# Optimization experiments

Hardware: AMD Instinct MI355X
Metric: run time of the kernel (lower is better)

## Reference

```python
import jax, jax.numpy as jnp
import numpy as np

B, XL, YL = 4, 128, 1024
D, H, L, DFF = 512, 8, 3, 2048
PV, AV, OV = 512, 1025, 1025
MASK_ID = 1024
EOS = 1024
DUR_W = 1.0
NEG = -1e9  # finite large-negative instead of -inf: keeps fully-padded rows NaN-free
HD = D // H
S = XL + 1 + YL


def sinusoid(n, d):
    pos = jnp.arange(n, dtype=jnp.float32)[:, None]
    div = jnp.exp(jnp.arange(0, d, 2, dtype=jnp.float32) * (-np.log(10000.0) / d))
    pe = jnp.zeros((n, d), dtype=jnp.float32)
    pe = pe.at[:, 0::2].set(jnp.sin(pos * div))
    pe = pe.at[:, 1::2].set(jnp.cos(pos * div))
    return pe


def layer_norm(x, g, b, eps=1e-5):
    mu = x.mean(-1, keepdims=True)
    var = ((x - mu) ** 2).mean(-1, keepdims=True)
    return (x - mu) * jax.lax.rsqrt(var + eps) * g + b


def setup_inputs():
    k = jax.random.split(jax.random.key(0), 32)
    x = jax.random.randint(k[0], (B, XL), 0, PV)
    x1_lens = jax.random.randint(k[1], (B,), 20, 60)
    x2_lens = jax.random.randint(k[2], (B,), 20, 60)
    y = jax.random.randint(k[3], (B, YL), 0, AV - 2)
    y1_lens = jax.random.randint(k[4], (B,), 100, 400)
    y2_lens = jax.random.randint(k[5], (B,), 300, 600)
    y_lens = y1_lens + 1 + y2_lens
    idx = jnp.arange(YL)[None, :]
    valid = (idx >= y1_lens[:, None] + 1) & (idx < y_lens[:, None] - 1)
    bern = jax.random.uniform(k[6], (B, YL)) < 0.3  # mask_ratio = mid(min,max)
    ym = bern & valid
    need = (~ym.any(1)) & valid.any(1)
    first = jnp.argmax(valid, axis=1)
    y_mask = ym | (need[:, None] & (idx == first[:, None]))
    emo_feature = jax.random.normal(k[7], (B, 768), dtype=jnp.float32)

    def n(kk, shape, s=0.02):
        return s * jax.random.normal(kk, shape, dtype=jnp.float32)

    inp = dict(x=x, x1_lens=x1_lens, x2_lens=x2_lens, y=y, y1_lens=y1_lens,
               y2_lens=y2_lens, y_mask=y_mask, emo_feature=emo_feature)
    inp['text_emb'] = n(k[8], (PV, D))
    inp['audio_emb'] = n(k[9], (AV, D))
    inp['type_emb'] = n(k[10], (3, D))
    inp['emo_W'] = n(k[11], (D, 768))
    inp['emo_b'] = jnp.zeros((D,), jnp.float32)
    inp['alpha_text'] = jnp.float32(1.0)
    inp['alpha_audio'] = jnp.float32(1.0)
    inp['Wqkv'] = n(k[12], (L, 3 * D, D))
    inp['bqkv'] = jnp.zeros((L, 3 * D), jnp.float32)
    inp['Wo'] = n(k[13], (L, D, D))
    inp['bo'] = jnp.zeros((L, D), jnp.float32)
    inp['ln1_g'] = jnp.ones((L, D), jnp.float32)
    inp['ln1_b'] = jnp.zeros((L, D), jnp.float32)
    inp['ln2_g'] = jnp.ones((L, D), jnp.float32)
    inp['ln2_b'] = jnp.zeros((L, D), jnp.float32)
    inp['W1'] = n(k[14], (L, DFF, D))
    inp['b1'] = jnp.zeros((L, DFF), jnp.float32)
    inp['W2'] = n(k[15], (L, D, DFF))
    inp['b2'] = jnp.zeros((L, D), jnp.float32)
    inp['predict_W'] = n(k[16], (OV, D))
    inp['dW1'] = n(k[17], (D // 2, D))
    inp['db1'] = jnp.zeros((D // 2,), jnp.float32)
    inp['dW2'] = n(k[18], (D // 4, D // 2))
    inp['db2'] = jnp.zeros((D // 4,), jnp.float32)
    inp['dW3'] = n(k[19], (1, D // 4))
    inp['db3'] = jnp.zeros((1,), jnp.float32)
    return inp


def build_attn_bias(x1_lens, x2_lens, y1_lens, y2_lens, y_mask):
    x_lens = x1_lens + 1 + x2_lens
    y_lens = y1_lens + 1 + y2_lens
    cS = jnp.arange(S)[None, :]  # [1,S] key columns
    # --- x rows ---
    rx = jnp.arange(XL)[None, :]
    is_x1 = rx < x1_lens[:, None]                                   # [B,XL]
    allow_x1 = cS < x1_lens[:, None]                                # [B,S]
    allow_x2 = (cS >= x1_lens[:, None]) & (cS < x_lens[:, None])
    x_allow = jnp.where(is_x1[:, :, None], allow_x1[:, None, :], allow_x2[:, None, :])
    # --- emo row: attends only to itself (col XL) ---
    emo_allow = jnp.broadcast_to((cS == XL)[:, None, :], (B, 1, S))
    # --- y rows ---
    ry = jnp.arange(YL)[None, :]
    is_y1 = ry < y1_lens[:, None]
    is_cls = ry == y1_lens[:, None]
    is_y2 = (ry > y1_lens[:, None]) & (ry < y_lens[:, None])
    allow_y1 = (cS < x1_lens[:, None]) | ((cS > XL) & (cS <= XL + y1_lens[:, None]))
    allow_cls = (cS < x_lens[:, None]) | (cS == XL) | ((cS > XL) & (cS <= XL + y1_lens[:, None] + 1))
    allow_y2 = (cS < x_lens[:, None]) | (cS == XL) | ((cS > XL) & (cS <= XL + y_lens[:, None]))
    ymask_full = jnp.zeros((B, S), bool).at[:, XL + 1:].set(y_mask)
    allow_y2 = allow_y2 & (~ymask_full)                             # masked tokens invisible
    y_allow = jnp.where(is_y1[:, :, None], allow_y1[:, None, :],
               jnp.where(is_cls[:, :, None], allow_cls[:, None, :],
                jnp.where(is_y2[:, :, None], allow_y2[:, None, :], False)))
    block = ~jnp.concatenate([x_allow, emo_allow, y_allow], axis=1)  # True = blocked
    return jnp.where(block, jnp.float32(NEG), jnp.float32(0.0))[:, None]  # [B,1,S,S]


def encoder_forward(h, bias, Wqkv, bqkv, Wo, bo, ln1_g, ln1_b, ln2_g, ln2_b, W1, b1, W2, b2):
    scale = 1.0 / np.sqrt(HD)
    for l in range(L):
        qkv = h @ Wqkv[l].T + bqkv[l]                               # [B,S,3D]
        q, k, v = jnp.split(qkv, 3, axis=-1)
        q = q.reshape(B, S, H, HD).transpose(0, 2, 1, 3)
        k = k.reshape(B, S, H, HD).transpose(0, 2, 1, 3)
        v = v.reshape(B, S, H, HD).transpose(0, 2, 1, 3)
        scores = jnp.einsum('bhqd,bhkd->bhqk', q, k) * scale + bias
        a = jax.nn.softmax(scores, axis=-1)
        o = jnp.einsum('bhqk,bhkd->bhqd', a, v).transpose(0, 2, 1, 3).reshape(B, S, D)
        o = o @ Wo[l].T + bo[l]
        h = layer_norm(h + o, ln1_g[l], ln1_b[l])                   # post-norm
        ff = jax.nn.relu(h @ W1[l].T + b1[l]) @ W2[l].T + b2[l]
        h = layer_norm(h + ff, ln2_g[l], ln2_b[l])
    return h


def reference(x, x1_lens, x2_lens, y, y1_lens, y2_lens, y_mask, emo_feature,
              text_emb, audio_emb, type_emb, emo_W, emo_b, alpha_text, alpha_audio,
              Wqkv, bqkv, Wo, bo, ln1_g, ln1_b, ln2_g, ln2_b, W1, b1, W2, b2,
              predict_W, dW1, db1, dW2, db2, dW3, db3):
    y_target = y
    x_emb = text_emb[x] + type_emb[0]
    x_pos = x_emb + alpha_text * sinusoid(XL, D)
    emo = emo_feature @ emo_W.T + emo_b + type_emb[1]
    y_in = jnp.where(y_mask, MASK_ID, y)
    y_emb = audio_emb[y_in] + type_emb[2]
    y_pos = y_emb + alpha_audio * sinusoid(YL, D)
    h_input = jnp.concatenate([x_pos, emo[:, None, :], y_pos], axis=1)  # [B,S,D]
    bias = build_attn_bias(x1_lens, x2_lens, y1_lens, y2_lens, y_mask)
    enc = encoder_forward(h_input, bias, Wqkv, bqkv, Wo, bo,
                          ln1_g, ln1_b, ln2_g, ln2_b, W1, b1, W2, b2)
    # duration loss on CLS hidden at prompt_lens = XL + 1 + y1_lens
    cls_hidden = enc[jnp.arange(B), XL + 1 + y1_lens]
    h1 = jax.nn.relu(cls_hidden @ dW1.T + db1)
    h2 = jax.nn.relu(h1 @ dW2.T + db2)
    pred_dur = (h2 @ dW3.T + db3)[:, 0]
    tgt_dur = y2_lens.astype(jnp.float32) / x2_lens.astype(jnp.float32)
    e = pred_dur - tgt_dur
    dur_loss = jnp.mean(jnp.where(jnp.abs(e) <= 1.0, 0.5 * e * e, jnp.abs(e) - 0.5))
    # token CE over masked positions (mean over masked tokens)
    logits = enc[:, XL + 1:] @ predict_W.T                          # [B,YL,OV]
    logp = jax.nn.log_softmax(logits, axis=-1)
    ce = -jnp.take_along_axis(logp, y_target[..., None], axis=-1)[..., 0]
    m = y_mask.astype(jnp.float32)
    token_loss = jnp.sum(ce * m) / jnp.sum(m)
    # top-3 accuracy ignoring EOS
    top3 = jax.lax.top_k(logits, 3)[1]
    correct = jnp.any(top3 == y_target[..., None], axis=-1)
    inc = (y_mask & (y_target != EOS)).astype(jnp.float32)
    acc = jnp.sum(correct.astype(jnp.float32) * inc) / jnp.maximum(jnp.sum(inc), 1.0)
    total_loss = token_loss + DUR_W * dur_loss
    return total_loss, acc
```

## Files before the change

### kernel.cpp

```cpp
#include <hip/hip_runtime.h>
#include <hip/hip_bf16.h>
#include <math.h>

#define BATCH 4
#define XL 128
#define YL 1024
#define DMODEL 512
#define NH 8
#define NLAYER 3
#define DFF 2048
#define MASK_ID 1024
#define EOS_TOK 1024
#define HD 64
#define SEQ 1153
#define OV 1025
#define NEGBIG (-1e9f)
#define QBLK 128
#define CCAP 2432
#define NROWS 36896

typedef unsigned short u16;
typedef unsigned int u32;
typedef short short8 __attribute__((ext_vector_type(8)));
typedef float f32x4 __attribute__((ext_vector_type(4)));

__device__ __forceinline__ u16 f2bf(float f) {
    union { float f; unsigned u; } v; v.f = f;
    unsigned r = v.u + 0x7fffu + ((v.u >> 16) & 1u);
    return (u16)(r >> 16);
}
__device__ __forceinline__ float bf2f(u16 b) {
    union { unsigned u; float f; } v; v.u = ((unsigned)b) << 16;
    return v.f;
}

__global__ __launch_bounds__(256) void cvt5_kernel(
    const float* __restrict__ s0, u16* __restrict__ d0, int n0,
    const float* __restrict__ s1, u16* __restrict__ d1, int n1,
    const float* __restrict__ s2, u16* __restrict__ d2, int n2,
    const float* __restrict__ s3, u16* __restrict__ d3, int n3,
    const float* __restrict__ s4, u16* __restrict__ d4, int n4)
{
    int c0 = n0, c1 = c0 + n1, c2 = c1 + n2, c3 = c2 + n3, c4 = c3 + n4;
    for (int i = blockIdx.x * 256 + threadIdx.x; i < c4; i += gridDim.x * 256) {
        const float* s; u16* d; int j;
        if (i < c0)      { s = s0; d = d0; j = i; }
        else if (i < c1) { s = s1; d = d1; j = i - c0; }
        else if (i < c2) { s = s2; d = d2; j = i - c1; }
        else if (i < c3) { s = s3; d = d3; j = i - c2; }
        else             { s = s4; d = d4; j = i - c3; }
        float4 v = ((const float4*)s)[j];
        ushort4 o;
        o.x = f2bf(v.x); o.y = f2bf(v.y); o.z = f2bf(v.z); o.w = f2bf(v.w);
        ((ushort4*)d)[j] = o;
    }
}

__global__ __launch_bounds__(256) void emo_kernel(
    const float* __restrict__ emo_feature, const float* __restrict__ emo_W,
    const float* __restrict__ emo_b, const float* __restrict__ type_emb,
    float* __restrict__ hbuf, u16* __restrict__ hbuf_bf)
{
    int b = blockIdx.x >> 3, c = blockIdx.x & 7;
    int t = threadIdx.x;
    int osub = t >> 2, ln = t & 3;
    int d = c * 64 + osub;
    const float* f = emo_feature + b * 768 + ln * 192;
    const float* w = emo_W + (size_t)d * 768 + ln * 192;
    float acc = 0.f;
    #pragma unroll 4
    for (int k = 0; k < 192; ++k) acc = fmaf(f[k], w[k], acc);
    acc += __shfl_xor(acc, 1);
    acc += __shfl_xor(acc, 2);
    if (ln == 0) {
        float v = acc + emo_b[d] + type_emb[DMODEL + d];
        hbuf[(size_t)(b * SEQ + XL) * DMODEL + d] = v;
        hbuf_bf[(size_t)(b * SEQ + XL) * DMODEL + d] = f2bf(v);
    }
}

__global__ __launch_bounds__(256) void build_h_kernel(
    const int* __restrict__ x, const int* __restrict__ y, const int* __restrict__ y_mask,
    const float* __restrict__ text_emb, const float* __restrict__ audio_emb,
    const float* __restrict__ type_emb,
    const float* __restrict__ alpha_text, const float* __restrict__ alpha_audio,
    float* __restrict__ hbuf, u16* __restrict__ hbuf_bf)
{
    int row = blockIdx.x * 4 + (threadIdx.x >> 6);
    int l = threadIdx.x & 63;
    int b = row / SEQ, s = row % SEQ;
    if (s == XL) return;
    int d0 = l * 8;

    const float* emb; const float* te; float alpha; int pos;
    if (s < XL) {
        int tok = x[b * XL + s];
        emb = text_emb + (size_t)tok * DMODEL;
        te = type_emb; alpha = alpha_text[0]; pos = s;
    } else {
        int r = s - XL - 1;
        int tok = y_mask[b * YL + r] ? MASK_ID : y[b * YL + r];
        emb = audio_emb + (size_t)tok * DMODEL;
        te = type_emb + 2 * DMODEL; alpha = alpha_audio[0]; pos = r;
    }

    float4 e0 = *(const float4*)(emb + d0);
    float4 e1 = *(const float4*)(emb + d0 + 4);
    float4 t0 = *(const float4*)(te + d0);
    float4 t1 = *(const float4*)(te + d0 + 4);
    float v[8] = {e0.x + t0.x, e0.y + t0.y, e0.z + t0.z, e0.w + t0.w,
                  e1.x + t1.x, e1.y + t1.y, e1.z + t1.z, e1.w + t1.w};
    float fp = (float)pos;
    #pragma unroll
    for (int p = 0; p < 4; ++p) {
        int d = d0 + 2 * p;
        float div = __expf((float)d * (-9.210340371976184f / (float)DMODEL));
        float sn, cs;
        __sincosf(fp * div, &sn, &cs);
        v[2 * p]     += alpha * sn;
        v[2 * p + 1] += alpha * cs;
    }

    float* hp = hbuf + (size_t)row * DMODEL + d0;
    *(float4*)hp       = make_float4(v[0], v[1], v[2], v[3]);
    *(float4*)(hp + 4) = make_float4(v[4], v[5], v[6], v[7]);
    short8 sv;
    #pragma unroll
    for (int e = 0; e < 8; ++e) sv[e] = (short)f2bf(v[e]);
    *(short8*)(hbuf_bf + (size_t)row * DMODEL + d0) = sv;
}

__global__ __launch_bounds__(512) void gemm_bf16_kernel(
    const u16* __restrict__ A, const u16* __restrict__ Bw,
    const float* __restrict__ bias,
    float* __restrict__ Cf, u16* __restrict__ Cb,
    int M, int N, int K, int relu)
{
    __shared__ u16 As[128 * 32];
    __shared__ u16 Bs[128 * 32];
    int tid = threadIdx.x;
    int w = tid >> 6, l = tid & 63;
    int m0 = blockIdx.y * 128, n0 = blockIdx.x * 128;
    int wm = (w >> 1) * 32, wn = (w & 1) * 64;

    f32x4 acc[2][4];
    #pragma unroll
    for (int i = 0; i < 2; ++i)
        #pragma unroll
        for (int j = 0; j < 4; ++j) acc[i][j] = (f32x4){0.f, 0.f, 0.f, 0.f};

    int srow = (w << 4) + (l >> 2);
    int skp = (l & 3) << 3;

    for (int k0 = 0; k0 < K; k0 += 32) {
        {
            int am = m0 + srow; if (am >= M) am = M - 1;
            int bn = n0 + srow; if (bn >= N) bn = N - 1;
            __builtin_amdgcn_global_load_lds(
                (const __attribute__((address_space(1))) void*)(A + (size_t)am * K + k0 + skp),
                (__attribute__((address_space(3))) void*)(As + (w << 9)), 16, 0, 0);
            __builtin_amdgcn_global_load_lds(
                (const __attribute__((address_space(1))) void*)(Bw + (size_t)bn * K + k0 + skp),
                (__attribute__((address_space(3))) void*)(Bs + (w << 9)), 16, 0, 0);
        }
        __syncthreads();
        short8 af[2], bfr[4];
        #pragma unroll
        for (int i = 0; i < 2; ++i)
            af[i]  = *(const short8*)(As + (wm + i * 16 + (l & 15)) * 32 + ((l >> 4) << 3));
        #pragma unroll
        for (int j = 0; j < 4; ++j)
            bfr[j] = *(const short8*)(Bs + (wn + j * 16 + (l & 15)) * 32 + ((l >> 4) << 3));
        #pragma unroll
        for (int i = 0; i < 2; ++i)
            #pragma unroll
            for (int j = 0; j < 4; ++j)
                acc[i][j] = __builtin_amdgcn_mfma_f32_16x16x32_bf16(af[i], bfr[j], acc[i][j], 0, 0, 0);
        __syncthreads();
    }

    #pragma unroll
    for (int i = 0; i < 2; ++i) {
        #pragma unroll
        for (int j = 0; j < 4; ++j) {
            #pragma unroll
            for (int jj = 0; jj < 4; ++jj) {
                int row = m0 + wm + i * 16 + ((l >> 4) << 2) + jj;
                int col = n0 + wn + j * 16 + (l & 15);
                if (row < M && col < N) {
                    float v = acc[i][j][jj];
                    if (bias) v += bias[col];
                    if (relu) v = fmaxf(v, 0.f);
                    if (Cf) Cf[(size_t)row * N + col] = v;
                    if (Cb) Cb[(size_t)row * N + col] = f2bf(v);
                }
            }
        }
    }
}

__global__ __launch_bounds__(512) void gemm_bf16_splitk_kernel(
    const u16* __restrict__ A, const u16* __restrict__ Bw,
    float* __restrict__ P0, float* __restrict__ P1, float* __restrict__ P2,
    int M, int N, int K, int klen)
{
    __shared__ u16 As[128 * 32];
    __shared__ u16 Bs[128 * 32];
    int tid = threadIdx.x;
    int w = tid >> 6, l = tid & 63;
    int z = blockIdx.z;
    float* Cp = (z == 0) ? P0 : (z == 1) ? P1 : P2;
    int kbeg = z * klen;
    int kend = min(kbeg + klen, K);
    int m0 = blockIdx.y * 128, n0 = blockIdx.x * 128;
    int wm = (w >> 1) * 32, wn = (w & 1) * 64;

    f32x4 acc[2][4];
    #pragma unroll
    for (int i = 0; i < 2; ++i)
        #pragma unroll
        for (int j = 0; j < 4; ++j) acc[i][j] = (f32x4){0.f, 0.f, 0.f, 0.f};

    int srow = (w << 4) + (l >> 2);
    int skp = (l & 3) << 3;

    for (int k0 = kbeg; k0 < kend; k0 += 32) {
        {
            int am = m0 + srow; if (am >= M) am = M - 1;
            int bn = n0 + srow; if (bn >= N) bn = N - 1;
            __builtin_amdgcn_global_load_lds(
                (const __attribute__((address_space(1))) void*)(A + (size_t)am * K + k0 + skp),
                (__attribute__((address_space(3))) void*)(As + (w << 9)), 16, 0, 0);
            __builtin_amdgcn_global_load_lds(
                (const __attribute__((address_space(1))) void*)(Bw + (size_t)bn * K + k0 + skp),
                (__attribute__((address_space(3))) void*)(Bs + (w << 9)), 16, 0, 0);
        }
        __syncthreads();
        short8 af[2], bfr[4];
        #pragma unroll
        for (int i = 0; i < 2; ++i)
            af[i]  = *(const short8*)(As + (wm + i * 16 + (l & 15)) * 32 + ((l >> 4) << 3));
        #pragma unroll
        for (int j = 0; j < 4; ++j)
            bfr[j] = *(const short8*)(Bs + (wn + j * 16 + (l & 15)) * 32 + ((l >> 4) << 3));
        #pragma unroll
        for (int i = 0; i < 2; ++i)
            #pragma unroll
            for (int j = 0; j < 4; ++j)
                acc[i][j] = __builtin_amdgcn_mfma_f32_16x16x32_bf16(af[i], bfr[j], acc[i][j], 0, 0, 0);
        __syncthreads();
    }

    #pragma unroll
    for (int i = 0; i < 2; ++i) {
        #pragma unroll
        for (int j = 0; j < 4; ++j) {
            #pragma unroll
            for (int jj = 0; jj < 4; ++jj) {
                int row = m0 + wm + i * 16 + ((l >> 4) << 2) + jj;
                int col = n0 + wn + j * 16 + (l & 15);
                if (row < M && col < N)
                    Cp[(size_t)row * N + col] = acc[i][j][jj];
            }
        }
    }
}

__global__ __launch_bounds__(512) void gemm_bf16_splitk_dynm_kernel(
    const u16* __restrict__ A, const u16* __restrict__ Bw,
    const int* __restrict__ Mp,
    float* __restrict__ P0, float* __restrict__ P1,
    int N, int K, int klen)
{
    int M = *Mp;
    int m0 = blockIdx.y * 128;
    if (m0 >= M) return;
    __shared__ u16 As[128 * 32];
    __shared__ u16 Bs[128 * 32];
    int tid = threadIdx.x;
    int w = tid >> 6, l = tid & 63;
    int z = blockIdx.z;
    float* Cp = (z == 0) ? P0 : P1;
    int kbeg = z * klen;
    int kend = min(kbeg + klen, K);
    int n0 = blockIdx.x * 128;
    int wm = (w >> 1) * 32, wn = (w & 1) * 64;

    f32x4 acc[2][4];
    #pragma unroll
    for (int i = 0; i < 2; ++i)
        #pragma unroll
        for (int j = 0; j < 4; ++j) acc[i][j] = (f32x4){0.f, 0.f, 0.f, 0.f};

    int srow = (w << 4) + (l >> 2);
    int skp = (l & 3) << 3;

    for (int k0 = kbeg; k0 < kend; k0 += 32) {
        {
            int am = m0 + srow; if (am >= M) am = M - 1;
            int bn = n0 + srow; if (bn >= N) bn = N - 1;
            __builtin_amdgcn_global_load_lds(
                (const __attribute__((address_space(1))) void*)(A + (size_t)am * K + k0 + skp),
                (__attribute__((address_space(3))) void*)(As + (w << 9)), 16, 0, 0);
            __builtin_amdgcn_global_load_lds(
                (const __attribute__((address_space(1))) void*)(Bw + (size_t)bn * K + k0 + skp),
                (__attribute__((address_space(3))) void*)(Bs + (w << 9)), 16, 0, 0);
        }
        __syncthreads();
        short8 af[2], bfr[4];
        #pragma unroll
        for (int i = 0; i < 2; ++i)
            af[i]  = *(const short8*)(As + (wm + i * 16 + (l & 15)) * 32 + ((l >> 4) << 3));
        #pragma unroll
        for (int j = 0; j < 4; ++j)
            bfr[j] = *(const short8*)(Bs + (wn + j * 16 + (l & 15)) * 32 + ((l >> 4) << 3));
        #pragma unroll
        for (int i = 0; i < 2; ++i)
            #pragma unroll
            for (int j = 0; j < 4; ++j)
                acc[i][j] = __builtin_amdgcn_mfma_f32_16x16x32_bf16(af[i], bfr[j], acc[i][j], 0, 0, 0);
        __syncthreads();
    }

    #pragma unroll
    for (int i = 0; i < 2; ++i) {
        #pragma unroll
        for (int j = 0; j < 4; ++j) {
            #pragma unroll
            for (int jj = 0; jj < 4; ++jj) {
                int row = m0 + wm + i * 16 + ((l >> 4) << 2) + jj;
                int col = n0 + wn + j * 16 + (l & 15);
                if (row < M && col < N)
                    Cp[(size_t)row * N + col] = acc[i][j][jj];
            }
        }
    }
}

__global__ __launch_bounds__(512) void attn_mfma_kernel(
    const u16* __restrict__ qkv,
    const int* __restrict__ x1_lens, const int* __restrict__ x2_lens,
    const int* __restrict__ y1_lens, const int* __restrict__ y2_lens,
    const int* __restrict__ y_mask,
    float* __restrict__ opart, float* __restrict__ ml)
{
    __shared__ u16 Ks[64 * 64];
    __shared__ u16 Vt[64 * 64];
    __shared__ unsigned long long Bits[7][19];

    int tid = threadIdx.x;
    int w = tid >> 6, l = tid & 63;
    int g = l >> 4;
    int q = l & 15;
    int bh = blockIdx.y;
    int b = bh >> 3, h = bh & 7;
    int q0 = blockIdx.x * QBLK;
    int z = blockIdx.z;

    int x1 = x1_lens[b], xlen = x1 + 1 + x2_lens[b];
    int y1 = y1_lens[b], ylen = y1 + 1 + y2_lens[b];

    int kmax = -1;
    if (q0 < XL) kmax = max(kmax, xlen - 1);
    if (XL >= q0 && XL < q0 + QBLK) kmax = max(kmax, XL);
    {
        int ry0 = max(0, q0 - XL - 1);
        int ry1 = min(YL - 1, q0 + QBLK - 2 - XL);
        if (ry0 <= ry1) {
            if (ry0 <= y1 - 1) kmax = max(kmax, XL + y1);
            if (y1 >= ry0 && y1 <= ry1) kmax = max(kmax, XL + y1 + 1);
            int a = max(ry0, y1 + 1), bb = min(ry1, ylen - 1);
            if (a <= bb) kmax = max(kmax, XL + ylen);
        }
    }
    if (kmax < 0) kmax = 0;
    int NKT = (kmax >> 6) + 1;
    int half = (NKT + 1) >> 1;
    int kbeg = z ? half : 0;
    int kend = z ? NKT : half;

    for (int pp = w; pp < 7 * 19; pp += 8) {
        int ty = pp / 19, tile = pp - ty * 19;
        int c = tile * 64 + l;
        bool allow = false;
        if (c < SEQ && ty < 6) {
            bool a2c = (c == XL), ygt = (c > XL);
            if (ty == 0) allow = (c < x1);
            else if (ty == 1) allow = (c >= x1) && (c < xlen);
            else if (ty == 2) allow = a2c;
            else if (ty == 3) allow = (c < x1) || (ygt && c <= XL + y1);
            else if (ty == 4) allow = (c < xlen) || a2c || (ygt && c <= XL + y1 + 1);
            else {
                int ym = ygt ? y_mask[b * YL + c - XL - 1] : 0;
                allow = (((c < xlen) || a2c || (ygt && c <= XL + ylen)) && !ym);
            }
        }
        unsigned long long mk = __ballot(allow);
        if (l == 0) Bits[ty][tile] = mk;
    }

    int qr = q0 + w * 16 + q;
    int qrc = min(qr, SEQ - 1);
    short8 qf0, qf1;
    {
        const u16* qp = qkv + (size_t)(b * SEQ + qrc) * 1536 + h * 64 + (g << 3);
        short8 r0 = *(const short8*)qp;
        short8 r1 = *(const short8*)(qp + 32);
        #pragma unroll
        for (int e = 0; e < 8; ++e) {
            qf0[e] = (short)f2bf(bf2f((u16)r0[e]) * 0.125f);
            qf1[e] = (short)f2bf(bf2f((u16)r1[e]) * 0.125f);
        }
    }

    int rt;
    {
        if (qr >= SEQ) rt = 6;
        else if (qr < XL) rt = (qr < x1) ? 0 : 1;
        else if (qr == XL) rt = 2;
        else {
            int ry = qr - XL - 1;
            rt = (ry < y1) ? 3 : (ry == y1) ? 4 : (ry < ylen) ? 5 : 6;
        }
    }

    f32x4 oacc[4];
    #pragma unroll
    for (int db = 0; db < 4; ++db) oacc[db] = (f32x4){0.f, 0.f, 0.f, 0.f};
    float mrun = -INFINITY, lrun = 0.f;

    int srcA = q + ((g & 1) << 5);
    int srcB = srcA + 16;
    bool hi = (g >> 1) & 1;

    for (int kt = kbeg; kt < kend; ++kt) {
        __syncthreads();
        {
            int r = tid >> 3, d0k = (tid & 7) << 3;
            int krc = min(kt * 64 + r, SEQ - 1);
            short8 ka = *(const short8*)(qkv + (size_t)(b * SEQ + krc) * 1536 + 512 + h * 64 + d0k);
            *(short8*)&Ks[r * 64 + (d0k ^ ((r & 7) << 3))] = ka;
        }
        {
            int rp = tid >> 4, o = tid & 15;
            int d0v = o * 4;
            int k0r = min(kt * 64 + 2 * rp, SEQ - 1);
            int k1r = min(kt * 64 + 2 * rp + 1, SEQ - 1);
            ushort4 va = *(const ushort4*)(qkv + (size_t)(b * SEQ + k0r) * 1536 + 1024 + h * 64 + d0v);
            ushort4 vb = *(const ushort4*)(qkv + (size_t)(b * SEQ + k1r) * 1536 + 1024 + h * 64 + d0v);
            u32 pv[4] = {(u32)va.x | ((u32)vb.x << 16), (u32)va.y | ((u32)vb.y << 16),
                         (u32)va.z | ((u32)vb.z << 16), (u32)va.w | ((u32)vb.w << 16)};
            #pragma unroll
            for (int e = 0; e < 4; ++e) {
                int d = d0v + e;
                *(u32*)&Vt[d * 64 + ((2 * rp) ^ ((d & 7) << 3))] = pv[e];
            }
        }
        __syncthreads();

        f32x4 sc[4];
        #pragma unroll
        for (int cb = 0; cb < 4; ++cb) {
            int krw = cb * 16 + q;
            int ksw = (krw & 7) << 3;
            short8 k0 = *(const short8*)&Ks[krw * 64 + ((g << 3) ^ ksw)];
            short8 k1 = *(const short8*)&Ks[krw * 64 + ((32 + (g << 3)) ^ ksw)];
            f32x4 zz = (f32x4){0.f, 0.f, 0.f, 0.f};
            zz = __builtin_amdgcn_mfma_f32_16x16x32_bf16(k0, qf0, zz, 0, 0, 0);
            sc[cb] = __builtin_amdgcn_mfma_f32_16x16x32_bf16(k1, qf1, zz, 0, 0, 0);
        }

        unsigned long long mb = Bits[rt][kt];
        #pragma unroll
        for (int cb = 0; cb < 4; ++cb) {
            unsigned nib = (unsigned)(mb >> (16 * cb + 4 * g)) & 0xFu;
            #pragma unroll
            for (int r = 0; r < 4; ++r)
                sc[cb][r] = ((nib >> r) & 1u) ? sc[cb][r] : NEGBIG;
        }

        float tmax = sc[0][0];
        #pragma unroll
        for (int cb = 0; cb < 4; ++cb)
            #pragma unroll
            for (int r = 0; r < 4; ++r) tmax = fmaxf(tmax, sc[cb][r]);
        tmax = fmaxf(tmax, __shfl_xor(tmax, 16));
        tmax = fmaxf(tmax, __shfl_xor(tmax, 32));
        float newm = fmaxf(mrun, tmax);
        float corr = __expf(mrun - newm);
        float p[4][4];
        float ps = 0.f;
        #pragma unroll
        for (int cb = 0; cb < 4; ++cb)
            #pragma unroll
            for (int r = 0; r < 4; ++r) {
                p[cb][r] = __expf(sc[cb][r] - newm);
                ps += p[cb][r];
            }
        ps += __shfl_xor(ps, 16);
        ps += __shfl_xor(ps, 32);
        lrun = lrun * corr + ps;
        mrun = newm;

        float cr[4];
        #pragma unroll
        for (int r = 0; r < 4; ++r) cr[r] = __shfl(corr, (g << 2) + r);
        #pragma unroll
        for (int db = 0; db < 4; ++db)
            #pragma unroll
            for (int r = 0; r < 4; ++r) oacc[db][r] *= cr[r];

        u32 P0[4], P1[4];
        #pragma unroll
        for (int cb = 0; cb < 4; ++cb) {
            P0[cb] = (u32)f2bf(p[cb][0]) | ((u32)f2bf(p[cb][1]) << 16);
            P1[cb] = (u32)f2bf(p[cb][2]) | ((u32)f2bf(p[cb][3]) << 16);
        }

        union { u32 u[4]; short8 s; } f1, f2;
        {
            u32 a0 = __shfl(P0[0], srcA), a1 = __shfl(P1[0], srcA);
            u32 a2 = __shfl(P0[0], srcB), a3 = __shfl(P1[0], srcB);
            u32 b0 = __shfl(P0[1], srcA), b1 = __shfl(P1[1], srcA);
            u32 b2 = __shfl(P0[1], srcB), b3 = __shfl(P1[1], srcB);
            f1.u[0] = hi ? b0 : a0; f1.u[1] = hi ? b1 : a1;
            f1.u[2] = hi ? b2 : a2; f1.u[3] = hi ? b3 : a3;
            u32 c0 = __shfl(P0[2], srcA), c1 = __shfl(P1[2], srcA);
            u32 c2 = __shfl(P0[2], srcB), c3 = __shfl(P1[2], srcB);
            u32 d0 = __shfl(P0[3], srcA), d1 = __shfl(P1[3], srcA);
            u32 d2 = __shfl(P0[3], srcB), d3 = __shfl(P1[3], srcB);
            f2.u[0] = hi ? d0 : c0; f2.u[1] = hi ? d1 : c1;
            f2.u[2] = hi ? d2 : c2; f2.u[3] = hi ? d3 : c3;
        }

        #pragma unroll
        for (int db = 0; db < 4; ++db) {
            int vr = db * 16 + q;
            int vsw = (vr & 7) << 3;
            short8 v0 = *(const short8*)&Vt[vr * 64 + ((g << 3) ^ vsw)];
            short8 v1 = *(const short8*)&Vt[vr * 64 + ((32 + (g << 3)) ^ vsw)];
            oacc[db] = __builtin_amdgcn_mfma_f32_16x16x32_bf16(f1.s, v0, oacc[db], 0, 0, 0);
            oacc[db] = __builtin_amdgcn_mfma_f32_16x16x32_bf16(f2.s, v1, oacc[db], 0, 0, 0);
        }
    }

    if (g == 0) {
        int row = q0 + w * 16 + q;
        if (row < SEQ) {
            int ridx = (b * SEQ + row) * 8 + h;
            ml[(size_t)(z * 2) * NROWS + ridx] = mrun;
            ml[(size_t)(z * 2 + 1) * NROWS + ridx] = lrun;
        }
    }
    float* op = opart + (size_t)z * NROWS * 64;
    #pragma unroll
    for (int db = 0; db < 4; ++db) {
        #pragma unroll
        for (int r = 0; r < 4; ++r) {
            int qrj = q0 + w * 16 + (g << 2) + r;
            if (qrj < SEQ) {
                int ridx = (b * SEQ + qrj) * 8 + h;
                op[(size_t)ridx * 64 + db * 16 + q] = oacc[db][r];
            }
        }
    }
}

__global__ __launch_bounds__(256) void attn_merge_kernel(
    const float* __restrict__ opart, const float* __restrict__ ml,
    u16* __restrict__ obuf)
{
    int r = blockIdx.x * 4 + (threadIdx.x >> 6);
    int d = threadIdx.x & 63;
    float m0 = ml[r], l0 = ml[NROWS + r];
    float m1 = ml[2 * NROWS + r], l1 = ml[3 * NROWS + r];
    float M = fmaxf(m0, m1);
    float w0 = __expf(m0 - M), w1 = __expf(m1 - M);
    float denom = w0 * l0 + w1 * l1;
    float o0 = opart[(size_t)r * 64 + d];
    float o1 = opart[(size_t)(NROWS + r) * 64 + d];
    float v = (w0 * o0 + w1 * o1) / denom;
    int bs = r >> 3, h = r & 7;
    obuf[(size_t)bs * DMODEL + h * 64 + d] = f2bf(v);
}

__global__ __launch_bounds__(256) void add_ln_kernel(
    float* __restrict__ hbuf, u16* __restrict__ hbuf_bf,
    const float* __restrict__ p0, const float* __restrict__ p1,
    const float* __restrict__ p2, const float* __restrict__ bias,
    const float* __restrict__ g, const float* __restrict__ beta)
{
    int row = blockIdx.x * 4 + (threadIdx.x >> 6);
    int l = threadIdx.x & 63;
    int d0 = l * 8;
    size_t off = (size_t)row * DMODEL + d0;
    float* hp = hbuf + off;
    float4 a0 = *(const float4*)hp, a1 = *(const float4*)(hp + 4);
    float4 q0 = *(const float4*)(p0 + off), q1 = *(const float4*)(p0 + off + 4);
    float v[8] = {a0.x + q0.x, a0.y + q0.y, a0.z + q0.z, a0.w + q0.w,
                  a1.x + q1.x, a1.y + q1.y, a1.z + q1.z, a1.w + q1.w};
    if (p1) {
        float4 r0 = *(const float4*)(p1 + off), r1 = *(const float4*)(p1 + off + 4);
        v[0] += r0.x; v[1] += r0.y; v[2] += r0.z; v[3] += r0.w;
        v[4] += r1.x; v[5] += r1.y; v[6] += r1.z; v[7] += r1.w;
    }
    if (p2) {
        float4 r0 = *(const float4*)(p2 + off), r1 = *(const float4*)(p2 + off + 4);
        v[0] += r0.x; v[1] += r0.y; v[2] += r0.z; v[3] += r0.w;
        v[4] += r1.x; v[5] += r1.y; v[6] += r1.z; v[7] += r1.w;
    }
    {
        float4 b0 = *(const float4*)(bias + d0), b1 = *(const float4*)(bias + d0 + 4);
        v[0] += b0.x; v[1] += b0.y; v[2] += b0.z; v[3] += b0.w;
        v[4] += b1.x; v[5] += b1.y; v[6] += b1.z; v[7] += b1.w;
    }
    float s = 0.f;
    #pragma unroll
    for (int e = 0; e < 8; ++e) s += v[e];
    #pragma unroll
    for (int off2 = 32; off2 > 0; off2 >>= 1) s += __shfl_xor(s, off2);
    float mu = s * (1.f / DMODEL);
    float sq = 0.f;
    #pragma unroll
    for (int e = 0; e < 8; ++e) { v[e] -= mu; sq += v[e] * v[e]; }
    #pragma unroll
    for (int off2 = 32; off2 > 0; off2 >>= 1) sq += __shfl_xor(sq, off2);
    float inv = 1.f / sqrtf(sq * (1.f / DMODEL) + 1e-5f);
    float4 g0 = *(const float4*)(g + d0), g1 = *(const float4*)(g + d0 + 4);
    float4 be0 = *(const float4*)(beta + d0), be1 = *(const float4*)(beta + d0 + 4);
    float o[8];
    o[0] = v[0] * inv * g0.x + be0.x; o[1] = v[1] * inv * g0.y + be0.y;
    o[2] = v[2] * inv * g0.z + be0.z; o[3] = v[3] * inv * g0.w + be0.w;
    o[4] = v[4] * inv * g1.x + be1.x; o[5] = v[5] * inv * g1.y + be1.y;
    o[6] = v[6] * inv * g1.z + be1.z; o[7] = v[7] * inv * g1.w + be1.w;
    *(float4*)hp       = make_float4(o[0], o[1], o[2], o[3]);
    *(float4*)(hp + 4) = make_float4(o[4], o[5], o[6], o[7]);
    short8 sv;
    #pragma unroll
    for (int e = 0; e < 8; ++e) sv[e] = (short)f2bf(o[e]);
    *(short8*)(hbuf_bf + off) = sv;
}

__global__ __launch_bounds__(256) void init_accum_kernel(float* accum) {
    if (threadIdx.x < 8) accum[threadIdx.x] = 0.f;
}

__global__ __launch_bounds__(256) void compact_kernel(
    const int* __restrict__ y_mask, int* __restrict__ cnt, int* __restrict__ cmap)
{
    int i = blockIdx.x * 256 + threadIdx.x;
    if (i < BATCH * YL && y_mask[i]) {
        int pos = atomicAdd(cnt, 1);
        cmap[pos] = i;
    }
}

__global__ __launch_bounds__(256) void copy_rows_kernel(
    const int* __restrict__ cnt, const int* __restrict__ cmap,
    const u16* __restrict__ hbuf_bf, const int* __restrict__ y,
    u16* __restrict__ cbuf, int* __restrict__ ctgt)
{
    int i = blockIdx.x;
    if (i >= *cnt) return;
    int g = cmap[i];
    int b = g >> 10, r = g & 1023;
    const u16* src = hbuf_bf + (size_t)(b * SEQ + XL + 1 + r) * DMODEL;
    u16* dst = cbuf + (size_t)i * DMODEL;
    int t = threadIdx.x;
    ((ushort2*)dst)[t] = ((const ushort2*)src)[t];
    if (t == 0) ctgt[i] = y[g];
}

__global__ __launch_bounds__(256) void ce_kernel(
    const int* __restrict__ cnt,
    const float* __restrict__ lg0, const float* __restrict__ lg1,
    const int* __restrict__ ctgt, float* __restrict__ accum)
{
    int row = blockIdx.x;
    if (row >= *cnt) return;
    const float* lp0 = lg0 + (size_t)row * OV;
    const float* lp1 = lg1 + (size_t)row * OV;
    int tgt = ctgt[row];
    int t = threadIdx.x;
    __shared__ float red[4];

    float lmax = -INFINITY;
    for (int i = t; i < OV; i += 256) lmax = fmaxf(lmax, lp0[i] + lp1[i]);
    #pragma unroll
    for (int off = 32; off > 0; off >>= 1) lmax = fmaxf(lmax, __shfl_xor(lmax, off));
    if ((t & 63) == 0) red[t >> 6] = lmax;
    __syncthreads();
    lmax = fmaxf(fmaxf(red[0], red[1]), fmaxf(red[2], red[3]));
    __syncthreads();

    float lsum = 0.f;
    for (int i = t; i < OV; i += 256) lsum += expf(lp0[i] + lp1[i] - lmax);
    #pragma unroll
    for (int off = 32; off > 0; off >>= 1) lsum += __shfl_xor(lsum, off);
    if ((t & 63) == 0) red[t >> 6] = lsum;
    __syncthreads();
    lsum = red[0] + red[1] + red[2] + red[3];
    __syncthreads();

    float lt = lp0[tgt] + lp1[tgt];
    float cntr = 0.f;
    for (int i = t; i < OV; i += 256) {
        float v = lp0[i] + lp1[i];
        if (v > lt || (v == lt && i < tgt)) cntr += 1.f;
    }
    #pragma unroll
    for (int off = 32; off > 0; off >>= 1) cntr += __shfl_xor(cntr, off);
    if ((t & 63) == 0) red[t >> 6] = cntr;
    __syncthreads();
    cntr = red[0] + red[1] + red[2] + red[3];

    if (t == 0) {
        float ce = -(lt - lmax - logf(lsum));
        float inc = (tgt != EOS_TOK) ? 1.f : 0.f;
        float corr = (cntr < 2.5f) ? 1.f : 0.f;
        atomicAdd(&accum[0], ce);
        atomicAdd(&accum[1], 1.f);
        atomicAdd(&accum[2], corr * inc);
        atomicAdd(&accum[3], inc);
    }
}

__global__ __launch_bounds__(256) void dur1_kernel(
    const float* __restrict__ hbuf, const int* __restrict__ y1_lens,
    const float* __restrict__ dW1, const float* __restrict__ db1,
    float* __restrict__ h1buf)
{
    __shared__ float cls[DMODEL];
    int g = blockIdx.x;
    int b = g >> 3, c = g & 7;
    int t = threadIdx.x;
    const float* cp = hbuf + (size_t)(b * SEQ + XL + 1 + y1_lens[b]) * DMODEL;
    cls[t] = cp[t]; cls[t + 256] = cp[t + 256];
    __syncthreads();
    int row = c * 32 + (t >> 3);
    int ln = t & 7;
    const float* w = dW1 + (size_t)row * DMODEL + ln * 64;
    const float* cv = cls + ln * 64;
    float acc = 0.f;
    #pragma unroll 8
    for (int k = 0; k < 64; ++k) acc = fmaf(cv[k], w[k], acc);
    acc += __shfl_xor(acc, 1); acc += __shfl_xor(acc, 2); acc += __shfl_xor(acc, 4);
    if (ln == 0) h1buf[b * 256 + row] = fmaxf(acc + db1[row], 0.f);
}

__global__ __launch_bounds__(256) void dur2_kernel(
    const float* __restrict__ h1buf,
    const float* __restrict__ dW2, const float* __restrict__ db2,
    const float* __restrict__ dW3, const float* __restrict__ db3,
    float* __restrict__ preds)
{
    __shared__ float h1s[256];
    __shared__ float h2s[128];
    int b = blockIdx.x;
    int t = threadIdx.x;
    h1s[t] = h1buf[b * 256 + t];
    __syncthreads();
    if (t < 128) {
        float acc = db2[t];
        const float* w = dW2 + (size_t)t * 256;
        for (int k = 0; k < 256; ++k) acc = fmaf(h1s[k], w[k], acc);
        h2s[t] = fmaxf(acc, 0.f);
    }
    __syncthreads();
    if (t < 64) {
        float v = h2s[t] * dW3[t] + h2s[t + 64] * dW3[t + 64];
        #pragma unroll
        for (int off = 32; off > 0; off >>= 1) v += __shfl_xor(v, off);
        if (t == 0) preds[b] = v + db3[0];
    }
}

__global__ __launch_bounds__(64) void final_kernel(
    const float* __restrict__ accum, const float* __restrict__ preds,
    const int* __restrict__ y2_lens, const int* __restrict__ x2_lens,
    float* __restrict__ out)
{
    if (threadIdx.x == 0) {
        float dl = 0.f;
        for (int b = 0; b < BATCH; ++b) {
            float tgt = (float)y2_lens[b] / (float)x2_lens[b];
            float e = preds[b] - tgt;
            float ae = fabsf(e);
            dl += (ae <= 1.f) ? 0.5f * e * e : (ae - 0.5f);
        }
        dl *= (1.f / BATCH);
        float token_loss = accum[0] / accum[1];
        float acc_v = accum[2] / fmaxf(accum[3], 1.f);
        out[0] = token_loss + dl;
        out[1] = acc_v;
    }
}

extern "C" void kernel_launch(void* const* d_in, const int* in_sizes, int n_in,
                              void* d_out, int out_size, void* d_ws, size_t ws_size,
                              hipStream_t stream)
{
    const int*   x           = (const int*)d_in[0];
    const int*   x1_lens     = (const int*)d_in[1];
    const int*   x2_lens     = (const int*)d_in[2];
    const int*   y           = (const int*)d_in[3];
    const int*   y1_lens     = (const int*)d_in[4];
    const int*   y2_lens     = (const int*)d_in[5];
    const int*   y_mask      = (const int*)d_in[6];
    const float* emo_feature = (const float*)d_in[7];
    const float* text_emb    = (const float*)d_in[8];
    const float* audio_emb   = (const float*)d_in[9];
    const float* type_emb    = (const float*)d_in[10];
    const float* emo_W       = (const float*)d_in[11];
    const float* emo_b       = (const float*)d_in[12];
    const float* alpha_text  = (const float*)d_in[13];
    const float* alpha_audio = (const float*)d_in[14];
    const float* Wqkv        = (const float*)d_in[15];
    const float* bqkv        = (const float*)d_in[16];
    const float* Wo          = (const float*)d_in[17];
    const float* bo          = (const float*)d_in[18];
    const float* ln1_g       = (const float*)d_in[19];
    const float* ln1_b       = (const float*)d_in[20];
    const float* ln2_g       = (const float*)d_in[21];
    const float* ln2_b       = (const float*)d_in[22];
    const float* W1          = (const float*)d_in[23];
    const float* b1          = (const float*)d_in[24];
    const float* W2          = (const float*)d_in[25];
    const float* b2          = (const float*)d_in[26];
    const float* predict_W   = (const float*)d_in[27];
    const float* dW1         = (const float*)d_in[28];
    const float* db1         = (const float*)d_in[29];
    const float* dW2         = (const float*)d_in[30];
    const float* db2         = (const float*)d_in[31];
    const float* dW3         = (const float*)d_in[32];
    const float* db3         = (const float*)d_in[33];

    const int M = BATCH * SEQ;
    char* p = (char*)d_ws;
    float* hbuf   = (float*)p; p += 9445376;
    float* delta  = (float*)p; p += 9445376;
    char*  uni    = p;         p += 18909440;
    u16*   hbuf_bf = (u16*)p;  p += 4722688;
    u16*   qkv_bf  = (u16*)p;  p += 14168064;
    u16*   obuf_bf = (u16*)p;  p += 4722688;
    u16*   wbf     = (u16*)p;  p += 19923968;
    u16*   cbuf    = (u16*)p;  p += (size_t)CCAP * DMODEL * 2;
    u16*   ff1_bf  = (u16*)uni;

    float* partA = (float*)qkv_bf;
    float* partB = (float*)((char*)qkv_bf + 9445376);
    float* lg0   = (float*)uni;
    float* lg1   = (float*)qkv_bf;
    float* opart = (float*)uni;
    float* mlbuf = delta;

    float* accum  = delta;
    int*   cnt    = (int*)(delta + 4);
    float* preds  = delta + 8;
    int*   cmap   = (int*)(delta + 16);
    int*   ctgt   = cmap + CCAP;
    float* h1buf  = (float*)(ctgt + CCAP);

    u16* wq_bf = wbf;
    u16* wo_bf = wq_bf + 2359296;
    u16* w1_bf = wo_bf + 786432;
    u16* w2_bf = w1_bf + 3145728;
    u16* wp_bf = w2_bf + 3145728;

    cvt5_kernel<<<1024, 256, 0, stream>>>(
        Wqkv, wq_bf, 2359296 / 4,
        Wo, wo_bf, 786432 / 4,
        W1, w1_bf, 3145728 / 4,
        W2, w2_bf, 3145728 / 4,
        predict_W, wp_bf, 524800 / 4);

    emo_kernel<<<32, 256, 0, stream>>>(emo_feature, emo_W, emo_b, type_emb, hbuf, hbuf_bf);
    build_h_kernel<<<M / 4, 256, 0, stream>>>(
        x, y, y_mask, text_emb, audio_emb, type_emb,
        alpha_text, alpha_audio, hbuf, hbuf_bf);

    const int MG = (M + 127) / 128;
    for (int l = 0; l < NLAYER; ++l) {
        gemm_bf16_kernel<<<dim3(12, MG), 512, 0, stream>>>(
            hbuf_bf, wq_bf + (size_t)l * 1536 * 512, bqkv + l * 1536,
            nullptr, qkv_bf, M, 1536, 512, 0);
        attn_mfma_kernel<<<dim3((SEQ + QBLK - 1) / QBLK, BATCH * NH, 2), 512, 0, stream>>>(
            qkv_bf, x1_lens, x2_lens, y1_lens, y2_lens, y_mask, opart, mlbuf);
        attn_merge_kernel<<<NROWS / 4, 256, 0, stream>>>(opart, mlbuf, obuf_bf);
        gemm_bf16_splitk_kernel<<<dim3(4, MG, 2), 512, 0, stream>>>(
            obuf_bf, wo_bf + (size_t)l * 512 * 512,
            delta, partA, nullptr, M, 512, 512, 256);
        add_ln_kernel<<<M / 4, 256, 0, stream>>>(hbuf, hbuf_bf,
            delta, partA, nullptr, bo + l * 512,
            ln1_g + l * DMODEL, ln1_b + l * DMODEL);
        gemm_bf16_kernel<<<dim3(16, MG), 512, 0, stream>>>(
            hbuf_bf, w1_bf + (size_t)l * 2048 * 512, b1 + l * 2048,
            nullptr, ff1_bf, M, 2048, 512, 1);
        gemm_bf16_splitk_kernel<<<dim3(4, MG, 3), 512, 0, stream>>>(
            ff1_bf, w2_bf + (size_t)l * 512 * 2048,
            delta, partA, partB, M, 512, 2048, 768);
        add_ln_kernel<<<M / 4, 256, 0, stream>>>(hbuf, hbuf_bf,
            delta, partA, partB, b2 + l * 512,
            ln2_g + l * DMODEL, ln2_b + l * DMODEL);
    }

    init_accum_kernel<<<1, 64, 0, stream>>>(accum);
    compact_kernel<<<(BATCH * YL) / 256, 256, 0, stream>>>(y_mask, cnt, cmap);
    copy_rows_kernel<<<CCAP, 256, 0, stream>>>(cnt, cmap, hbuf_bf, y, cbuf, ctgt);
    gemm_bf16_splitk_dynm_kernel<<<dim3((OV + 127) / 128, CCAP / 128, 2), 512, 0, stream>>>(
        cbuf, wp_bf, cnt, lg0, lg1, OV, 512, 256);
    ce_kernel<<<CCAP, 256, 0, stream>>>(cnt, lg0, lg1, ctgt, accum);

    dur1_kernel<<<32, 256, 0, stream>>>(hbuf, y1_lens, dW1, db1, h1buf);
    dur2_kernel<<<4, 256, 0, stream>>>(h1buf, dW2, db2, dW3, db3, preds);
    final_kernel<<<1, 64, 0, stream>>>(accum, preds, y2_lens, x2_lens, (float*)d_out);
}
```

Measured before the change: 527.7 us.

## Fuse split-K attention merge into attention kernel via intra-block wave groups

The key-range split moves from a separate grid dimension into two 4-wave groups inside each block, using a 64-row query tile. Each group stages its own K/V tile in shared memory. The groups merge their partial softmax states through shared memory before writing bf16 output directly. This removes the separate merge kernel and the fp32 partial-output round trip through global memory. It also reverses block order so the longest query tiles launch first, at the cost of idle iterations for the group with fewer key tiles and more shared memory per block.

```diff
diff --git a/kernel.cpp b/kernel.cpp
--- a/kernel.cpp
+++ b/kernel.cpp
@@ -15,9 +15,8 @@
 #define SEQ 1153
 #define OV 1025
 #define NEGBIG (-1e9f)
-#define QBLK 128
+#define QBLK 64
 #define CCAP 2432
-#define NROWS 36896
 
 typedef unsigned short u16;
 typedef unsigned int u32;
@@ -342,20 +341,24 @@
     const int* __restrict__ x1_lens, const int* __restrict__ x2_lens,
     const int* __restrict__ y1_lens, const int* __restrict__ y2_lens,
     const int* __restrict__ y_mask,
-    float* __restrict__ opart, float* __restrict__ ml)
-{
-    __shared__ u16 Ks[64 * 64];
-    __shared__ u16 Vt[64 * 64];
+    u16* __restrict__ obuf)
+{
+    __shared__ u16 Ks[2][64 * 64];
+    __shared__ u16 Vt[2][64 * 64];
     __shared__ unsigned long long Bits[7][19];
+    __shared__ float Om[4][16][65];
+    __shared__ float MLm[4][2][16];
 
     int tid = threadIdx.x;
     int w = tid >> 6, l = tid & 63;
+    int grp = w >> 2;
+    int wq = w & 3;
+    int ti = tid & 255;
     int g = l >> 4;
     int q = l & 15;
     int bh = blockIdx.y;
     int b = bh >> 3, h = bh & 7;
-    int q0 = blockIdx.x * QBLK;
-    int z = blockIdx.z;
+    int q0 = (gridDim.x - 1 - blockIdx.x) * QBLK;
 
     int x1 = x1_lens[b], xlen = x1 + 1 + x2_lens[b];
     int y1 = y1_lens[b], ylen = y1 + 1 + y2_lens[b];
@@ -375,9 +378,9 @@
     }
     if (kmax < 0) kmax = 0;
     int NKT = (kmax >> 6) + 1;
-    int half = (NKT + 1) >> 1;
-    int kbeg = z ? half : 0;
-    int kend = z ? NKT : half;
+    int h0 = (NKT + 1) >> 1;
+    int kbeg = grp ? h0 : 0;
+    int kend = grp ? NKT : h0;
 
     for (int pp = w; pp < 7 * 19; pp += 8) {
         int ty = pp / 19, tile = pp - ty * 19;
@@ -399,7 +402,7 @@
         if (l == 0) Bits[ty][tile] = mk;
     }
 
-    int qr = q0 + w * 16 + q;
+    int qr = q0 + wq * 16 + q;
     int qrc = min(qr, SEQ - 1);
     short8 qf0, qf1;
     {
@@ -433,38 +436,47 @@
     int srcB = srcA + 16;
     bool hi = (g >> 1) & 1;
 
-    for (int kt = kbeg; kt < kend; ++kt) {
+    for (int i = 0; i < h0; ++i) {
+        int kt = kbeg + i;
+        bool act = kt < kend;
         __syncthreads();
-        {
-            int r = tid >> 3, d0k = (tid & 7) << 3;
-            int krc = min(kt * 64 + r, SEQ - 1);
-            short8 ka = *(const short8*)(qkv + (size_t)(b * SEQ + krc) * 1536 + 512 + h * 64 + d0k);
-            *(short8*)&Ks[r * 64 + (d0k ^ ((r & 7) << 3))] = ka;
-        }
-        {
-            int rp = tid >> 4, o = tid & 15;
-            int d0v = o * 4;
-            int k0r = min(kt * 64 + 2 * rp, SEQ - 1);
-            int k1r = min(kt * 64 + 2 * rp + 1, SEQ - 1);
-            ushort4 va = *(const ushort4*)(qkv + (size_t)(b * SEQ + k0r) * 1536 + 1024 + h * 64 + d0v);
-            ushort4 vb = *(const ushort4*)(qkv + (size_t)(b * SEQ + k1r) * 1536 + 1024 + h * 64 + d0v);
-            u32 pv[4] = {(u32)va.x | ((u32)vb.x << 16), (u32)va.y | ((u32)vb.y << 16),
-                         (u32)va.z | ((u32)vb.z << 16), (u32)va.w | ((u32)vb.w << 16)};
-            #pragma unroll
-            for (int e = 0; e < 4; ++e) {
-                int d = d0v + e;
-                *(u32*)&Vt[d * 64 + ((2 * rp) ^ ((d & 7) << 3))] = pv[e];
+        if (act) {
+            #pragma unroll
+            for (int ii = 0; ii < 2; ++ii) {
+                int idx = ti + (ii << 8);
+                int r = idx >> 3, d0k = (idx & 7) << 3;
+                int krc = min(kt * 64 + r, SEQ - 1);
+                short8 ka = *(const short8*)(qkv + (size_t)(b * SEQ + krc) * 1536 + 512 + h * 64 + d0k);
+                *(short8*)&Ks[grp][r * 64 + (d0k ^ ((r & 7) << 3))] = ka;
             }
+            #pragma unroll
+            for (int ii = 0; ii < 2; ++ii) {
+                int idx = ti + (ii << 8);
+                int rp = idx >> 4, o = idx & 15;
+                int d0v = o * 4;
+                int k0r = min(kt * 64 + 2 * rp, SEQ - 1);
+                int k1r = min(kt * 64 + 2 * rp + 1, SEQ - 1);
+                ushort4 va = *(const ushort4*)(qkv + (size_t)(b * SEQ + k0r) * 1536 + 1024 + h * 64 + d0v);
+                ushort4 vb = *(const ushort4*)(qkv + (size_t)(b * SEQ + k1r) * 1536 + 1024 + h * 64 + d0v);
+                u32 pv[4] = {(u32)va.x | ((u32)vb.x << 16), (u32)va.y | ((u32)vb.y << 16),
+                             (u32)va.z | ((u32)vb.z << 16), (u32)va.w | ((u32)vb.w << 16)};
+                #pragma unroll
+                for (int e = 0; e < 4; ++e) {
+                    int d = d0v + e;
+                    *(u32*)&Vt[grp][d * 64 + ((2 * rp) ^ ((d & 7) << 3))] = pv[e];
+                }
+            }
         }
         __syncthreads();
+        if (!act) continue;
 
         f32x4 sc[4];
         #pragma unroll
         for (int cb = 0; cb < 4; ++cb) {
             int krw = cb * 16 + q;
             int ksw = (krw & 7) << 3;
-            short8 k0 = *(const short8*)&Ks[krw * 64 + ((g << 3) ^ ksw)];
-            short8 k1 = *(const short8*)&Ks[krw * 64 + ((32 + (g << 3)) ^ ksw)];
+            short8 k0 = *(const short8*)&Ks[grp][krw * 64 + ((g << 3) ^ ksw)];
+            short8 k1 = *(const short8*)&Ks[grp][krw * 64 + ((32 + (g << 3)) ^ ksw)];
             f32x4 zz = (f32x4){0.f, 0.f, 0.f, 0.f};
             zz = __builtin_amdgcn_mfma_f32_16x16x32_bf16(k0, qf0, zz, 0, 0, 0);
             sc[cb] = __builtin_amdgcn_mfma_f32_16x16x32_bf16(k1, qf1, zz, 0, 0, 0);
@@ -537,51 +549,49 @@
         for (int db = 0; db < 4; ++db) {
             int vr = db * 16 + q;
             int vsw = (vr & 7) << 3;
-            short8 v0 = *(const short8*)&Vt[vr * 64 + ((g << 3) ^ vsw)];
-            short8 v1 = *(const short8*)&Vt[vr * 64 + ((32 + (g << 3)) ^ vsw)];
+            short8 v0 = *(const short8*)&Vt[grp][vr * 64 + ((g << 3) ^ vsw)];
+            short8 v1 = *(const short8*)&Vt[grp][vr * 64 + ((32 + (g << 3)) ^ vsw)];
             oacc[db] = __builtin_amdgcn_mfma_f32_16x16x32_bf16(f1.s, v0, oacc[db], 0, 0, 0);
             oacc[db] = __builtin_amdgcn_mfma_f32_16x16x32_bf16(f2.s, v1, oacc[db], 0, 0, 0);
         }
     }
 
-    if (g == 0) {
-        int row = q0 + w * 16 + q;
-        if (row < SEQ) {
-            int ridx = (b * SEQ + row) * 8 + h;
-            ml[(size_t)(z * 2) * NROWS + ridx] = mrun;
-            ml[(size_t)(z * 2 + 1) * NROWS + ridx] = lrun;
-        }
-    }
-    float* op = opart + (size_t)z * NROWS * 64;
-    #pragma unroll
-    for (int db = 0; db < 4; ++db) {
+    __syncthreads();
+    if (grp == 1) {
+        #pragma unroll
+        for (int db = 0; db < 4; ++db)
+            #pragma unroll
+            for (int r = 0; r < 4; ++r)
+                Om[wq][(g << 2) + r][db * 16 + q] = oacc[db][r];
+        if (g == 0) { MLm[wq][0][q] = mrun; MLm[wq][1][q] = lrun; }
+    }
+    __syncthreads();
+    if (grp == 0) {
+        float mB = MLm[wq][0][q], lB = MLm[wq][1][q];
+        float M = fmaxf(mrun, mB);
+        float wA = __expf(mrun - M), wB = __expf(mB - M);
+        float denom = wA * lrun + wB * lB;
+        float wAr[4], wBr[4], dr[4];
         #pragma unroll
         for (int r = 0; r < 4; ++r) {
-            int qrj = q0 + w * 16 + (g << 2) + r;
-            if (qrj < SEQ) {
-                int ridx = (b * SEQ + qrj) * 8 + h;
-                op[(size_t)ridx * 64 + db * 16 + q] = oacc[db][r];
+            int src = (g << 2) + r;
+            wAr[r] = __shfl(wA, src);
+            wBr[r] = __shfl(wB, src);
+            dr[r]  = 1.f / __shfl(denom, src);
+        }
+        #pragma unroll
+        for (int db = 0; db < 4; ++db) {
+            #pragma unroll
+            for (int r = 0; r < 4; ++r) {
+                int qrj = q0 + wq * 16 + (g << 2) + r;
+                if (qrj < SEQ) {
+                    float ov = (wAr[r] * oacc[db][r] +
+                                wBr[r] * Om[wq][(g << 2) + r][db * 16 + q]) * dr[r];
+                    obuf[(size_t)(b * SEQ + qrj) * DMODEL + h * 64 + db * 16 + q] = f2bf(ov);
+                }
             }
         }
     }
-}
-
-__global__ __launch_bounds__(256) void attn_merge_kernel(
-    const float* __restrict__ opart, const float* __restrict__ ml,
-    u16* __restrict__ obuf)
-{
-    int r = blockIdx.x * 4 + (threadIdx.x >> 6);
-    int d = threadIdx.x & 63;
-    float m0 = ml[r], l0 = ml[NROWS + r];
-    float m1 = ml[2 * NROWS + r], l1 = ml[3 * NROWS + r];
-    float M = fmaxf(m0, m1);
-    float w0 = __expf(m0 - M), w1 = __expf(m1 - M);
-    float denom = w0 * l0 + w1 * l1;
-    float o0 = opart[(size_t)r * 64 + d];
-    float o1 = opart[(size_t)(NROWS + r) * 64 + d];
-    float v = (w0 * o0 + w1 * o1) / denom;
-    int bs = r >> 3, h = r & 7;
-    obuf[(size_t)bs * DMODEL + h * 64 + d] = f2bf(v);
 }
 
 __global__ __launch_bounds__(256) void add_ln_kernel(
@@ -851,8 +861,6 @@
     float* partB = (float*)((char*)qkv_bf + 9445376);
     float* lg0   = (float*)uni;
     float* lg1   = (float*)qkv_bf;
-    float* opart = (float*)uni;
-    float* mlbuf = delta;
 
     float* accum  = delta;
     int*   cnt    = (int*)(delta + 4);
@@ -884,9 +892,8 @@
         gemm_bf16_kernel<<<dim3(12, MG), 512, 0, stream>>>(
             hbuf_bf, wq_bf + (size_t)l * 1536 * 512, bqkv + l * 1536,
             nullptr, qkv_bf, M, 1536, 512, 0);
-        attn_mfma_kernel<<<dim3((SEQ + QBLK - 1) / QBLK, BATCH * NH, 2), 512, 0, stream>>>(
-            qkv_bf, x1_lens, x2_lens, y1_lens, y2_lens, y_mask, opart, mlbuf);
-        attn_merge_kernel<<<NROWS / 4, 256, 0, stream>>>(opart, mlbuf, obuf_bf);
+        attn_mfma_kernel<<<dim3((SEQ + QBLK - 1) / QBLK, BATCH * NH), 512, 0, stream>>>(
+            qkv_bf, x1_lens, x2_lens, y1_lens, y2_lens, y_mask, obuf_bf);
         gemm_bf16_splitk_kernel<<<dim3(4, MG, 2), 512, 0, stream>>>(
             obuf_bf, wo_bf + (size_t)l * 512 * 512,
             delta, partA, nullptr, M, 512, 512, 256);
```

New measurement: 519.6 us (median of 2 runs). About the same (-1.5%).
